# Kernel tuning notes

Hardware: AMD Instinct MI355X
Metric: run time of the kernel (lower is better)

## Reference

```python
import jax, jax.numpy as jnp
import numpy as np

TOPK = 2


def setup_inputs() -> dict:
    key = jax.random.key(0)
    ks = jax.random.split(key, 6)
    B, S, D, H, M = 2, 2048, 256, 8, 8
    s = 0.02
    return {
        "x": jax.random.normal(ks[0], (B, S, D), jnp.float32),
        "Wq": jax.random.normal(ks[1], (D, H * D), jnp.float32) * s,
        "bq": jnp.zeros((H * D,), jnp.float32),
        "Wr": jax.random.normal(ks[2], (D, M), jnp.float32) * s,
        "br": jnp.zeros((M,), jnp.float32),
        "Wk": jax.random.normal(ks[3], (M, D, H * D), jnp.float32) * s,
        "bk": jnp.zeros((M, H * D), jnp.float32),
        "Wv": jax.random.normal(ks[4], (M, D, H * D), jnp.float32) * s,
        "bv": jnp.zeros((M, H * D), jnp.float32),
        "Wo": jax.random.normal(ks[5], (H * D, D), jnp.float32) * s,
        "bo": jnp.zeros((D,), jnp.float32),
        "bias0": jnp.zeros((B, M), jnp.float32),
    }


def reference(x, Wq, bq, Wr, br, Wk, bk, Wv, bv, Wo, bo, bias0):
    B, S, D = x.shape
    M, _, HD = Wk.shape
    H = HD // D
    # query projection and head split: [B,S,H,D] (head dim == n_text_state)
    q = (x @ Wq + bq).reshape(B, S, H, D)
    # router + aux-loss-free bias-adjusted top-k routing (DeepSeek-V3 style)
    scores = jax.nn.softmax(x @ Wr + br, axis=-1)                 # [B,S,M]
    biased = scores + bias0[:, None, :]
    _, idx = jax.lax.top_k(biased, TOPK)                          # [B,S,TOPK]
    mask = jax.nn.one_hot(idx, M, dtype=scores.dtype).sum(-2)     # [B,S,M] in {0,1}
    routing = scores * mask
    routing = routing / routing.sum(-1, keepdims=True)
    # per-memory linear-attention state: M_m = sum_s r[b,s,m] * k (x) v, fused over all memories
    k_all = (jnp.einsum('bsd,mde->mbse', x, Wk) + bk[:, None, None, :]).reshape(M, B, S, H, D)
    v_all = (jnp.einsum('bsd,mde->mbse', x, Wv) + bv[:, None, None, :]).reshape(M, B, S, H, D)
    mem = jnp.einsum('bsm,mbshk,mbshv->bhkv', routing, k_all, v_all)  # [B,H,D,D]
    # fused read-out (replaces per-timestep python loop): o[b,s,h,v] = sum_k mem[b,h,k,v] q[b,s,h,k]
    o = jnp.einsum('bhkv,bshk->bshv', mem, q)                     # [B,S,H,D]
    return o.reshape(B, S, H * D) @ Wo + bo
```

## Files before the change

kernel.cpp:

```cpp
#include <hip/hip_runtime.h>

typedef __attribute__((ext_vector_type(8))) short bf16x8;
typedef __attribute__((ext_vector_type(4))) float f32x4;

#define DEV static __device__ __forceinline__

DEV unsigned short f2bf(float f){
  union { float f; unsigned u; } v; v.f = f;
  unsigned r = v.u + 0x7fffu + ((v.u >> 16) & 1u);
  return (unsigned short)(r >> 16);
}
DEV float bf2f(unsigned short u){
  union { unsigned u; float f; } v; v.u = ((unsigned)u) << 16;
  return v.f;
}
DEV unsigned long long pk4(float a, float b, float c, float d){
  unsigned lo = (unsigned)f2bf(a) | ((unsigned)f2bf(b) << 16);
  unsigned hi = (unsigned)f2bf(c) | ((unsigned)f2bf(d) << 16);
  return ((unsigned long long)hi << 32) | lo;
}

__global__ __launch_bounds__(256) void k_prep(const float* __restrict__ x,
                                              const float* __restrict__ Wq,
                                              const float* __restrict__ Wr,
                                              const float* __restrict__ br,
                                              const float* __restrict__ Wk,
                                              const float* __restrict__ Wv,
                                              const float* __restrict__ Wo,
                                              const float* __restrict__ bias0,
                                              unsigned short* __restrict__ WkT,
                                              unsigned short* __restrict__ WvT,
                                              unsigned short* __restrict__ WoT,
                                              unsigned short* __restrict__ Wqb,
                                              unsigned short* __restrict__ xb,
                                              unsigned short* __restrict__ xT,
                                              float* __restrict__ routT){
  __shared__ float tile[32*33];
  __shared__ float lg[32][8];
  __shared__ float rt2[32][8];
  int bid = blockIdx.x;
  int t = threadIdx.x;
  int tx = t & 31, ty = t >> 5;

  if (bid < 8192){
    const float* src = (bid < 4096) ? Wk : Wv;
    unsigned short* dst = (bid < 4096) ? WkT : WvT;
    int q = bid & 4095;
    int bat = q >> 9, rem = q & 511;
    int c0 = (rem >> 3) * 32, r0 = (rem & 7) * 32;
    size_t boff = (size_t)bat * 256 * 2048;
    for (int i = 0; i < 4; i++)
      tile[(ty + i*8)*33 + tx] = src[boff + (size_t)(r0 + ty + i*8) * 2048 + c0 + tx];
    __syncthreads();
    for (int i = 0; i < 4; i++)
      dst[boff + (size_t)(c0 + ty + i*8) * 256 + r0 + tx] = f2bf(tile[tx*33 + ty + i*8]);
  } else if (bid < 8704){
    int q = bid - 8192;
    int c0 = (q >> 6) * 32, r0 = (q & 63) * 32;
    for (int i = 0; i < 4; i++)
      tile[(ty + i*8)*33 + tx] = Wo[(size_t)(r0 + ty + i*8) * 256 + c0 + tx];
    __syncthreads();
    for (int i = 0; i < 4; i++)
      WoT[(size_t)(c0 + ty + i*8) * 2048 + r0 + tx] = f2bf(tile[tx*33 + ty + i*8]);
  } else if (bid < 8960){
    int q = bid - 8704;
    size_t idx = (size_t)q * 2048 + t * 8;
    f32x4 a = *(const f32x4*)(Wq + idx);
    f32x4 b = *(const f32x4*)(Wq + idx + 4);
    *(unsigned long long*)(Wqb + idx)     = pk4(a[0], a[1], a[2], a[3]);
    *(unsigned long long*)(Wqb + idx + 4) = pk4(b[0], b[1], b[2], b[3]);
  } else if (bid < 9984){
    int q = bid - 8960;
    int bat = q >> 9, rem = q & 511;
    int c0 = (rem >> 6) * 32, r0 = (rem & 63) * 32;
    size_t boff = (size_t)bat * 2048 * 256;
    for (int i = 0; i < 4; i++){
      float v = x[boff + (size_t)(r0 + ty + i*8) * 256 + c0 + tx];
      tile[(ty + i*8)*33 + tx] = v;
      xb[boff + (size_t)(r0 + ty + i*8) * 256 + c0 + tx] = f2bf(v);
    }
    __syncthreads();
    for (int i = 0; i < 4; i++)
      xT[(size_t)(bat*256 + c0 + ty + i*8) * 2048 + r0 + tx] = f2bf(tile[tx*33 + ty + i*8]);
  } else {
    int row = t >> 3, mm = t & 7;
    int n = (bid - 9984) * 32 + row;
    const float* xr = x + (size_t)n * 256;
    float acc = 0.f;
    for (int d = 0; d < 256; d++) acc += xr[d] * Wr[d * 8 + mm];
    acc += br[mm];
    lg[row][mm] = acc;
    __syncthreads();
    if (t < 32){
      int r = t; int n2 = (bid - 9984) * 32 + r; int b = n2 >> 11;
      float mx = -1e30f;
      for (int i = 0; i < 8; i++) mx = fmaxf(mx, lg[r][i]);
      float s[8]; float sum = 0.f;
      for (int i = 0; i < 8; i++){ s[i] = __expf(lg[r][i] - mx); sum += s[i]; }
      for (int i = 0; i < 8; i++) s[i] /= sum;
      float bb[8];
      for (int i = 0; i < 8; i++) bb[i] = s[i] + bias0[b * 8 + i];
      int i1 = 0;
      for (int i = 1; i < 8; i++) if (bb[i] > bb[i1]) i1 = i;
      int i2 = -1;
      for (int i = 0; i < 8; i++){ if (i == i1) continue; if (i2 < 0 || bb[i] > bb[i2]) i2 = i; }
      float wsum = s[i1] + s[i2];
      for (int i = 0; i < 8; i++)
        rt2[r][i] = (i == i1) ? s[i1] / wsum : ((i == i2) ? s[i2] / wsum : 0.f);
    }
    __syncthreads();
    int n3 = (bid - 9984) * 32 + row;
    int b = n3 >> 11, sl = n3 & 2047;
    routT[((size_t)b * 8 + mm) * 2048 + sl] = rt2[row][mm];
  }
}

__global__ __launch_bounds__(256) void k_usum(const unsigned short* __restrict__ xb,
                                              const float* __restrict__ routT,
                                              float* __restrict__ upart, float* __restrict__ rhop){
  __shared__ float rl[128];
  int bid = blockIdx.x;
  int sc = bid & 15, bm = bid >> 4, b = bm >> 3;
  int t = threadIdx.x;
  int s0 = sc * 128;
  if (t < 128) rl[t] = routT[(size_t)bm * 2048 + s0 + t];
  __syncthreads();
  float acc = 0.f;
  const unsigned short* xrow = xb + ((size_t)(b * 2048 + s0)) * 256 + t;
  for (int s = 0; s < 128; s++){
    float rv = rl[s];
    if (rv != 0.f)
      acc += rv * bf2f(xrow[(size_t)s * 256]);
  }
  upart[(size_t)bid * 256 + t] = acc;
  if (t == 0){
    float rs = 0.f;
    for (int s = 0; s < 128; s++) rs += rl[s];
    rhop[bid] = rs;
  }
}

__global__ __launch_bounds__(256) void k_bias(const unsigned short* __restrict__ WkT,
                                              const unsigned short* __restrict__ WvT,
                                              const float* __restrict__ upart,
                                              const float* __restrict__ rhop,
                                              float* __restrict__ ku_g, float* __restrict__ vu_g,
                                              float* __restrict__ rho){
  __shared__ float uL[256];
  int bid = blockIdx.x, t = threadIdx.x;
  int bm = bid >> 3, hseg = bid & 7, m = bm & 7;
  {
    float s = 0.f;
    for (int scn = 0; scn < 16; scn++)
      s += upart[(size_t)(bm*16 + scn) * 256 + t];
    uL[t] = s;
  }
  if (hseg == 0 && t == 0){
    float rs = 0.f;
    for (int scn = 0; scn < 16; scn++) rs += rhop[bm*16 + scn];
    rho[bm] = rs;
  }
  __syncthreads();
  int hd = hseg * 256 + t;
  const unsigned short* wk = WkT + ((size_t)m*2048 + hd) * 256;
  const unsigned short* wv = WvT + ((size_t)m*2048 + hd) * 256;
  float sk = 0.f, sv = 0.f;
  for (int d8 = 0; d8 < 256; d8 += 8){
    bf16x8 a = *(const bf16x8*)(wk + d8);
    bf16x8 c = *(const bf16x8*)(wv + d8);
    for (int j = 0; j < 8; j++){
      sk += bf2f((unsigned short)a[j]) * uL[d8+j];
      sv += bf2f((unsigned short)c[j]) * uL[d8+j];
    }
  }
  ku_g[(size_t)bm*2048 + hd] = sk;
  vu_g[(size_t)bm*2048 + hd] = sv;
}

__global__ __launch_bounds__(512) void k_gpart(const unsigned short* __restrict__ xT,
                                               const float* __restrict__ routT,
                                               unsigned short* __restrict__ Gp){
  __shared__ unsigned short As[256*72];
  __shared__ unsigned short Bs[256*72];
  __shared__ float rl[64];
  int bid = blockIdx.x;
  int kc = bid & 7, m = (bid >> 3) & 7, b = bid >> 6;
  int bm = b * 8 + m;
  int t = threadIdx.x, lane = t & 63, w = t >> 6;
  int li = lane & 15, lgp = lane >> 4;
  int p = w >> 2, q = w & 3;
  f32x4 acc[8][4];
  for (int i = 0; i < 8; i++) for (int j = 0; j < 4; j++) acc[i][j] = (f32x4){0,0,0,0};
  for (int c4 = 0; c4 < 4; c4++){
    int s0 = kc * 256 + c4 * 64;
    if (t < 64) rl[t] = routT[(size_t)bm*2048 + s0 + t];
    __syncthreads();
    for (int qq = 0; qq < 4; qq++){
      int idx = t + qq*512;
      int row = idx >> 3, sc = (idx & 7) * 8;
      bf16x8 xv = *(const bf16x8*)(xT + ((size_t)(b*256 + row))*2048 + s0 + sc);
      *(bf16x8*)(&Bs[row*72 + sc]) = xv;
      f32x4 r0 = *(const f32x4*)(rl + sc);
      f32x4 r1 = *(const f32x4*)(rl + sc + 4);
      bf16x8 sv;
      sv[0]=(short)f2bf(bf2f((unsigned short)xv[0])*r0[0]);
      sv[1]=(short)f2bf(bf2f((unsigned short)xv[1])*r0[1]);
      sv[2]=(short)f2bf(bf2f((unsigned short)xv[2])*r0[2]);
      sv[3]=(short)f2bf(bf2f((unsigned short)xv[3])*r0[3]);
      sv[4]=(short)f2bf(bf2f((unsigned short)xv[4])*r1[0]);
      sv[5]=(short)f2bf(bf2f((unsigned short)xv[5])*r1[1]);
      sv[6]=(short)f2bf(bf2f((unsigned short)xv[6])*r1[2]);
      sv[7]=(short)f2bf(bf2f((unsigned short)xv[7])*r1[3]);
      *(bf16x8*)(&As[row*72 + sc]) = sv;
    }
    __syncthreads();
    for (int kk = 0; kk < 2; kk++){
      bf16x8 Bf[4];
      for (int j = 0; j < 4; j++)
        Bf[j] = *(const bf16x8*)(&Bs[(q*64 + j*16 + li)*72 + kk*32 + lgp*8]);
      for (int i = 0; i < 8; i++){
        bf16x8 Af = *(const bf16x8*)(&As[(p*128 + i*16 + li)*72 + kk*32 + lgp*8]);
        for (int j = 0; j < 4; j++)
          acc[i][j] = __builtin_amdgcn_mfma_f32_16x16x32_bf16(Af, Bf[j], acc[i][j], 0, 0, 0);
      }
    }
    __syncthreads();
  }
  unsigned short* Cs = As;
  for (int ph = 0; ph < 4; ph++){
    if (q == ph){
      for (int i = 0; i < 8; i++)
        for (int j = 0; j < 4; j++){
          int rr = j*16 + li, cc = p*128 + i*16 + lgp*4;
          *(unsigned long long*)(&Cs[rr*264 + cc]) =
            pk4(acc[i][j][0], acc[i][j][1], acc[i][j][2], acc[i][j][3]);
        }
    }
    __syncthreads();
    for (int qq = 0; qq < 4; qq++){
      int idx = t + qq*512;
      int row = idx >> 5, cc = (idx & 31) * 8;
      *(bf16x8*)(Gp + (((size_t)bm*8 + kc) << 16) + (size_t)(ph*64 + row)*256 + cc) =
        *(const bf16x8*)(&Cs[row*264 + cc]);
    }
    __syncthreads();
  }
}

__global__ __launch_bounds__(256) void k_gred(const unsigned short* __restrict__ Gp,
                                              unsigned short* __restrict__ G){
  int idx = blockIdx.x * 256 + threadIdx.x;
  int bm = idx >> 13; size_t e8 = (size_t)(idx & 8191) * 8;
  float s[8] = {0,0,0,0,0,0,0,0};
  for (int kc = 0; kc < 8; kc++){
    bf16x8 v = *(const bf16x8*)(Gp + (((size_t)bm*8 + kc) << 16) + e8);
    for (int j = 0; j < 8; j++) s[j] += bf2f((unsigned short)v[j]);
  }
  *(unsigned long long*)(G + ((size_t)bm << 16) + e8)     = pk4(s[0], s[1], s[2], s[3]);
  *(unsigned long long*)(G + ((size_t)bm << 16) + e8 + 4) = pk4(s[4], s[5], s[6], s[7]);
}

__global__ __launch_bounds__(512) void k_tmat(const unsigned short* __restrict__ G,
                                              const unsigned short* __restrict__ WvT,
                                              unsigned short* __restrict__ Tt){
  __shared__ unsigned short Cs[64*264];
  int bid = blockIdx.x;
  int hseg = bid & 15, bm = bid >> 4, m = bm & 7;
  int t = threadIdx.x, lane = t & 63, w = t >> 6;
  int li = lane & 15, lgp = lane >> 4;
  int r = w >> 1, c = w & 1;
  f32x4 acc[4][4];
  for (int i = 0; i < 4; i++) for (int j = 0; j < 4; j++) acc[i][j] = (f32x4){0,0,0,0};
  const unsigned short* gp = G + ((size_t)bm << 16) + (size_t)(r*64 + li)*256 + lgp*8;
  const unsigned short* wp = WvT + ((size_t)m*2048 + hseg*128 + c*64 + li)*256 + lgp*8;
  #pragma unroll
  for (int kk = 0; kk < 8; kk++){
    bf16x8 Bf[4];
    for (int j = 0; j < 4; j++)
      Bf[j] = *(const bf16x8*)(wp + (size_t)(j*16)*256 + kk*32);
    for (int i = 0; i < 4; i++){
      bf16x8 Af = *(const bf16x8*)(gp + (size_t)(i*16)*256 + kk*32);
      for (int j = 0; j < 4; j++)
        acc[i][j] = __builtin_amdgcn_mfma_f32_16x16x32_bf16(Af, Bf[j], acc[i][j], 0, 0, 0);
    }
  }
  for (int ph = 0; ph < 2; ph++){
    if (c == ph){
      for (int i = 0; i < 4; i++)
        for (int j = 0; j < 4; j++)
          *(unsigned long long*)(&Cs[(j*16 + li)*264 + r*64 + i*16 + lgp*4]) =
            pk4(acc[i][j][0], acc[i][j][1], acc[i][j][2], acc[i][j][3]);
    }
    __syncthreads();
    for (int q = 0; q < 4; q++){
      int idx = t + q*512;
      int row = idx >> 5, cc = (idx & 31) * 8;
      *(bf16x8*)(Tt + ((size_t)bm*2048 + hseg*128 + ph*64 + row)*256 + cc) =
        *(const bf16x8*)(&Cs[row*264 + cc]);
    }
    __syncthreads();
  }
}

__global__ __launch_bounds__(512) void k_kmat3(const unsigned short* __restrict__ Tt,
                                               const unsigned short* __restrict__ WkT,
                                               float* __restrict__ mempartF){
  int bid = blockIdx.x;
  int m = bid & 7, kq = (bid >> 3) & 1, vq = (bid >> 4) & 1, bh = bid >> 5;
  int b = bh >> 3, h = bh & 7;
  int hd0 = h * 256;
  int t = threadIdx.x, lane = t & 63, w = t >> 6;
  int li = lane & 15, lgp = lane >> 4;
  int wr = w >> 2, wc = w & 3;
  f32x4 acc[2][4];
  for (int i = 0; i < 2; i++) for (int j = 0; j < 4; j++) acc[i][j] = (f32x4){0,0,0,0};
  const unsigned short* ap = WkT + ((size_t)m*2048 + hd0 + kq*128 + wc*32 + li)*256 + lgp*8;
  const unsigned short* bp = Tt + ((size_t)(b*8 + m)*2048 + hd0 + vq*128 + wr*64 + li)*256 + lgp*8;
  #pragma unroll
  for (int kk = 0; kk < 8; kk++){
    bf16x8 Af[2], Bf[4];
    Af[0] = *(const bf16x8*)(ap + kk*32);
    Af[1] = *(const bf16x8*)(ap + 16*256 + kk*32);
    for (int j = 0; j < 4; j++)
      Bf[j] = *(const bf16x8*)(bp + (size_t)(j*16)*256 + kk*32);
    for (int i = 0; i < 2; i++)
      for (int j = 0; j < 4; j++)
        acc[i][j] = __builtin_amdgcn_mfma_f32_16x16x32_bf16(Af[i], Bf[j], acc[i][j], 0, 0, 0);
  }
  float* Fp = mempartF + ((((size_t)(m*16 + bh))*2 + vq)*2 + kq) * 16384;
  for (int j = 0; j < 4; j++){
    int vdt = wr*64 + j*16 + li;
    for (int i = 0; i < 2; i++){
      int kdt = wc*32 + i*16 + lgp*4;
      *(f32x4*)(Fp + (size_t)vdt*128 + kdt) = acc[i][j];
    }
  }
}

__global__ __launch_bounds__(256) void k_kred(const float* __restrict__ mempartF,
                                              const float* __restrict__ bk,
                                              const float* __restrict__ bv,
                                              const float* __restrict__ ku_g,
                                              const float* __restrict__ vu_g,
                                              const float* __restrict__ rho,
                                              unsigned short* __restrict__ memT){
  int idx = blockIdx.x * 256 + threadIdx.x;
  int bh = idx >> 14;
  int rem = idx & 16383;
  int vd = rem >> 6, kd = (rem & 63) * 4;
  int b = bh >> 3, h = bh & 7;
  int vdg = h*256 + vd, kdg = h*256 + kd;
  int vq = vd >> 7, kq = kd >> 7;
  size_t src = ((((size_t)bh)*2 + vq)*2 + kq) * 16384 + (size_t)(vd & 127)*128 + (kd & 127);
  f32x4 s = (f32x4){0,0,0,0};
  #pragma unroll
  for (int m = 0; m < 8; m++){
    f32x4 v = *(const f32x4*)(mempartF + (size_t)m*16*65536 + src);
    s[0] += v[0]; s[1] += v[1]; s[2] += v[2]; s[3] += v[3];
  }
  #pragma unroll
  for (int m = 0; m < 8; m++){
    float bvv = bv[(size_t)m*2048 + vdg];
    float bb  = vu_g[(size_t)(b*8+m)*2048 + vdg] + rho[b*8+m]*bvv;
    f32x4 ku4 = *(const f32x4*)(ku_g + (size_t)(b*8+m)*2048 + kdg);
    f32x4 bk4 = *(const f32x4*)(bk + (size_t)m*2048 + kdg);
    s[0] += ku4[0]*bvv + bk4[0]*bb;
    s[1] += ku4[1]*bvv + bk4[1]*bb;
    s[2] += ku4[2]*bvv + bk4[2]*bb;
    s[3] += ku4[3]*bvv + bk4[3]*bb;
  }
  *(unsigned long long*)(memT + (size_t)bh*65536 + (size_t)vd*256 + kd) =
    pk4(s[0], s[1], s[2], s[3]);
}

__global__ __launch_bounds__(512) void k_emat(const unsigned short* __restrict__ memT,
                                              const unsigned short* __restrict__ Wqb,
                                              const float* __restrict__ bq,
                                              unsigned short* __restrict__ Eb,
                                              float* __restrict__ qbAll){
  __shared__ unsigned short Cs[16*264];
  int bid = blockIdx.x;
  int dseg = bid & 3, bh = bid >> 2;
  int b = bh >> 3, h = bh & 7;
  int hd0 = h * 256, d0 = dseg * 64;
  int t = threadIdx.x, lane = t & 63, w = t >> 6;
  int li = lane & 15, lgp = lane >> 4;
  int r = w >> 2, c = w & 3;
  f32x4 acc[8];
  for (int i = 0; i < 8; i++) acc[i] = (f32x4){0,0,0,0};
  for (int kk = 0; kk < 8; kk++){
    bf16x8 Bf = *(const bf16x8*)(Wqb + (size_t)(d0 + c*16 + li)*2048 + hd0 + kk*32 + lgp*8);
    for (int i = 0; i < 8; i++){
      bf16x8 Af = *(const bf16x8*)(memT + (size_t)bh*65536 + (size_t)(r*128 + i*16 + li)*256 + kk*32 + lgp*8);
      acc[i] = __builtin_amdgcn_mfma_f32_16x16x32_bf16(Af, Bf, acc[i], 0, 0, 0);
    }
  }
  if (dseg == 0 && t < 256){
    const unsigned short* mrow = memT + (size_t)bh*65536 + (size_t)t*256;
    float s = 0.f;
    for (int k8 = 0; k8 < 256; k8 += 8){
      bf16x8 v = *(const bf16x8*)(mrow + k8);
      for (int e = 0; e < 8; e++) s += bf2f((unsigned short)v[e]) * bq[hd0 + k8 + e];
    }
    qbAll[(size_t)b*2048 + hd0 + t] = s;
  }
  for (int ph = 0; ph < 4; ph++){
    if (c == ph){
      for (int i = 0; i < 8; i++)
        *(unsigned long long*)(&Cs[li*264 + r*128 + i*16 + lgp*4]) =
          pk4(acc[i][0], acc[i][1], acc[i][2], acc[i][3]);
    }
    __syncthreads();
    {
      int row = t >> 5, cc = (t & 31) * 8;
      *(bf16x8*)(Eb + (size_t)b*524288 + (size_t)(d0 + ph*16 + row)*2048 + hd0 + cc) =
        *(const bf16x8*)(&Cs[row*264 + cc]);
    }
    __syncthreads();
  }
}

__global__ __launch_bounds__(512) void k_fmat(const unsigned short* __restrict__ Eb,
                                              const unsigned short* __restrict__ WoT,
                                              const float* __restrict__ qbAll,
                                              const float* __restrict__ bo,
                                              float* __restrict__ Fpart,
                                              float* __restrict__ c0acc){
  __shared__ float qL[2048];
  int bid = blockIdx.x;
  int t = threadIdx.x;
  if (bid >= 256){
    int b = bid - 256;
    for (int i = t; i < 2048; i += 512) qL[i] = qbAll[(size_t)b * 2048 + i];
    __syncthreads();
    int w = t >> 6, lane = t & 63;
    for (int dd = w; dd < 256; dd += 8){
      const unsigned short* wrow = WoT + (size_t)dd * 2048 + lane * 8;
      const float* qp = qL + lane * 8;
      float s = 0.f;
      for (int pass = 0; pass < 4; pass++){
        bf16x8 v = *(const bf16x8*)(wrow + pass * 512);
        const float* q = qp + pass * 512;
        for (int e = 0; e < 8; e++) s += bf2f((unsigned short)v[e]) * q[e];
      }
      for (int off = 32; off; off >>= 1) s += __shfl_down(s, off);
      if (lane == 0) c0acc[(size_t)b * 256 + dd] = s + bo[dd];
    }
    return;
  }
  int ks = bid & 7, dseg = (bid >> 3) & 3, doseg = (bid >> 5) & 3, b = bid >> 7;
  int do0 = doseg * 64, d0 = dseg * 64, k0 = ks * 256;
  int lane = t & 63, w = t >> 6;
  int li = lane & 15, lgp = lane >> 4;
  int r = w >> 2, c = w & 3;
  f32x4 acc[2];
  acc[0] = (f32x4){0,0,0,0}; acc[1] = (f32x4){0,0,0,0};
  const unsigned short* bp = Eb + (size_t)b*524288 + (size_t)(d0 + c*16 + li)*2048 + k0 + lgp*8;
  const unsigned short* ap = WoT + (size_t)(do0 + r*32 + li)*2048 + k0 + lgp*8;
  #pragma unroll
  for (int kk = 0; kk < 8; kk++){
    bf16x8 Bf = *(const bf16x8*)(bp + kk*32);
    bf16x8 Af0 = *(const bf16x8*)(ap + kk*32);
    bf16x8 Af1 = *(const bf16x8*)(ap + kk*32 + 16*2048);
    acc[0] = __builtin_amdgcn_mfma_f32_16x16x32_bf16(Af0, Bf, acc[0], 0, 0, 0);
    acc[1] = __builtin_amdgcn_mfma_f32_16x16x32_bf16(Af1, Bf, acc[1], 0, 0, 0);
  }
  int dd = d0 + c*16 + li;
  float* Fp = Fpart + ((size_t)(ks*2 + b)) * 65536;
  for (int i = 0; i < 2; i++){
    int dor = do0 + r*32 + i*16 + lgp*4;
    float* p = Fp + (size_t)dor*256 + dd;
    p[0]   = acc[i][0];
    p[256] = acc[i][1];
    p[512] = acc[i][2];
    p[768] = acc[i][3];
  }
}

__global__ __launch_bounds__(256) void k_fred(const float* __restrict__ Fpart,
                                              unsigned short* __restrict__ Fb){
  int idx = blockIdx.x * 256 + threadIdx.x;
  int b = idx >> 14; int e4 = (idx & 16383) * 4;
  f32x4 s = (f32x4){0,0,0,0};
  for (int ks = 0; ks < 8; ks++){
    f32x4 v = *(const f32x4*)(Fpart + ((size_t)(ks*2 + b)) * 65536 + e4);
    s[0] += v[0]; s[1] += v[1]; s[2] += v[2]; s[3] += v[3];
  }
  *(unsigned long long*)(Fb + (size_t)b*65536 + e4) = pk4(s[0], s[1], s[2], s[3]);
}

__global__ __launch_bounds__(512) void k_final2(const unsigned short* __restrict__ Fb,
                                                const unsigned short* __restrict__ xb,
                                                const float* __restrict__ c0acc,
                                                float* __restrict__ out){
  int bid = blockIdx.x;
  int tc = bid & 31, b = bid >> 5;
  int t = threadIdx.x, lane = t & 63, w = t >> 6;
  int li = lane & 15, lgp = lane >> 4;
  int r = w >> 1, c = w & 1;
  int tok0 = b * 2048 + tc * 64;
  f32x4 acc[4][2];
  for (int i = 0; i < 4; i++) for (int j = 0; j < 2; j++) acc[i][j] = (f32x4){0,0,0,0};
  for (int kk = 0; kk < 8; kk++){
    bf16x8 Bf[2];
    for (int j = 0; j < 2; j++)
      Bf[j] = *(const bf16x8*)(xb + (size_t)(tok0 + c*32 + j*16 + li)*256 + kk*32 + lgp*8);
    for (int i = 0; i < 4; i++){
      bf16x8 af = *(const bf16x8*)(Fb + (size_t)b*65536 + (size_t)(r*64 + i*16 + li)*256 + kk*32 + lgp*8);
      for (int j = 0; j < 2; j++)
        acc[i][j] = __builtin_amdgcn_mfma_f32_16x16x32_bf16(af, Bf[j], acc[i][j], 0, 0, 0);
    }
  }
  for (int i = 0; i < 4; i++){
    int dol = r*64 + i*16 + lgp*4;
    f32x4 c4 = *(const f32x4*)(c0acc + (size_t)b*256 + dol);
    for (int j = 0; j < 2; j++){
      int tokl = c*32 + j*16 + li;
      f32x4 v = acc[i][j];
      v[0] += c4[0]; v[1] += c4[1]; v[2] += c4[2]; v[3] += c4[3];
      *(f32x4*)(out + (size_t)(tok0 + tokl)*256 + dol) = v;
    }
  }
}

extern "C" void kernel_launch(void* const* d_in, const int* in_sizes, int n_in,
                              void* d_out, int out_size, void* d_ws, size_t ws_size,
                              hipStream_t stream) {
  const float* x     = (const float*)d_in[0];
  const float* Wq    = (const float*)d_in[1];
  const float* bq    = (const float*)d_in[2];
  const float* Wr    = (const float*)d_in[3];
  const float* br    = (const float*)d_in[4];
  const float* Wk    = (const float*)d_in[5];
  const float* bk    = (const float*)d_in[6];
  const float* Wv    = (const float*)d_in[7];
  const float* bv    = (const float*)d_in[8];
  const float* Wo    = (const float*)d_in[9];
  const float* bo    = (const float*)d_in[10];
  const float* bias0 = (const float*)d_in[11];
  float* out = (float*)d_out;

  char* ws = (char*)d_ws;
  size_t off = 0;
  auto alloc = [&](size_t bytes) -> char* {
    char* p = ws + off;
    off = (off + bytes + 255) & ~(size_t)255;
    return p;
  };
  unsigned short* xb   = (unsigned short*)alloc((size_t)4096 * 256 * 2);
  unsigned short* xT   = (unsigned short*)alloc((size_t)2 * 256 * 2048 * 2);
  unsigned short* Wqb  = (unsigned short*)alloc((size_t)256 * 2048 * 2);
  unsigned short* WkT  = (unsigned short*)alloc((size_t)8 * 2048 * 256 * 2);
  unsigned short* WvT  = (unsigned short*)alloc((size_t)8 * 2048 * 256 * 2);
  unsigned short* WoT  = (unsigned short*)alloc((size_t)256 * 2048 * 2);
  float*          routT= (float*)alloc((size_t)16 * 2048 * 4);
  float*          upart= (float*)alloc((size_t)256 * 256 * 4);
  float*          rhop = (float*)alloc((size_t)256 * 4);
  float*          rho  = (float*)alloc((size_t)16 * 4);
  float*          ku_g = (float*)alloc((size_t)16 * 2048 * 4);
  float*          vu_g = (float*)alloc((size_t)16 * 2048 * 4);
  unsigned short* Gp   = (unsigned short*)alloc((size_t)16 * 8 * 65536 * 2);
  unsigned short* G    = (unsigned short*)alloc((size_t)16 * 65536 * 2);
  unsigned short* memT = (unsigned short*)alloc((size_t)16 * 65536 * 2);
  unsigned short* Eb   = (unsigned short*)alloc((size_t)2 * 256 * 2048 * 2);
  float*          qbAll= (float*)alloc((size_t)2 * 2048 * 4);
  float*          Fpart= (float*)alloc((size_t)16 * 65536 * 4);
  unsigned short* Fb   = (unsigned short*)alloc((size_t)2 * 65536 * 2);
  float*          c0acc= (float*)alloc((size_t)2 * 256 * 4);
  float*          mempartF = (float*)alloc((size_t)8 * 16 * 65536 * 4);
  unsigned short* Tt   = Gp;
  (void)ws_size; (void)in_sizes; (void)n_in; (void)out_size;

  k_prep<<<10112, 256, 0, stream>>>(x, Wq, Wr, br, Wk, Wv, Wo, bias0,
                                    WkT, WvT, WoT, Wqb, xb, xT, routT);
  k_usum<<<256, 256, 0, stream>>>(xb, routT, upart, rhop);
  k_bias<<<128, 256, 0, stream>>>(WkT, WvT, upart, rhop, ku_g, vu_g, rho);
  k_gpart<<<128, 512, 0, stream>>>(xT, routT, Gp);
  k_gred<<<512, 256, 0, stream>>>(Gp, G);
  k_tmat<<<256, 512, 0, stream>>>(G, WvT, Tt);
  k_kmat3<<<512, 512, 0, stream>>>(Tt, WkT, mempartF);
  k_kred<<<1024, 256, 0, stream>>>(mempartF, bk, bv, ku_g, vu_g, rho, memT);
  k_emat<<<64, 512, 0, stream>>>(memT, Wqb, bq, Eb, qbAll);
  k_fmat<<<258, 512, 0, stream>>>(Eb, WoT, qbAll, bo, Fpart, c0acc);
  k_fred<<<128, 256, 0, stream>>>(Fpart, Fb);
  k_final2<<<64, 512, 0, stream>>>(Fb, xb, c0acc, out);
}
```

Measured before the change: 208.2 us.

## Enlarge prep transpose tiles, share WkT loads across batches, store partials in bf16

The prep kernel's transpose blocks now handle 64x64 tiles instead of 32x32, cutting the block count roughly fourfold. k_kmat3 now computes both batches in one block, so each WkT fragment is loaded once and reused for two MFMA streams, halving the grid. The per-memory partial sums are written as bf16 instead of fp32, halving the traffic between k_kmat3 and k_kred. The cost is extra rounding error in the eight-way partial sum and higher register pressure in k_kmat3.

```diff
diff --git a/kernel.cpp b/kernel.cpp
--- a/kernel.cpp
+++ b/kernel.cpp
@@ -35,56 +35,56 @@
                                               unsigned short* __restrict__ xb,
                                               unsigned short* __restrict__ xT,
                                               float* __restrict__ routT){
-  __shared__ float tile[32*33];
+  __shared__ float tile[64*65];
   __shared__ float lg[32][8];
   __shared__ float rt2[32][8];
   int bid = blockIdx.x;
   int t = threadIdx.x;
-  int tx = t & 31, ty = t >> 5;
-
-  if (bid < 8192){
-    const float* src = (bid < 4096) ? Wk : Wv;
-    unsigned short* dst = (bid < 4096) ? WkT : WvT;
-    int q = bid & 4095;
-    int bat = q >> 9, rem = q & 511;
-    int c0 = (rem >> 3) * 32, r0 = (rem & 7) * 32;
+  int tx = t & 63, ty = t >> 6;
+
+  if (bid < 2048){
+    const float* src = (bid < 1024) ? Wk : Wv;
+    unsigned short* dst = (bid < 1024) ? WkT : WvT;
+    int q = bid & 1023;
+    int bat = q >> 7, rem = q & 127;
+    int c0 = (rem >> 2) * 64, r0 = (rem & 3) * 64;
     size_t boff = (size_t)bat * 256 * 2048;
-    for (int i = 0; i < 4; i++)
-      tile[(ty + i*8)*33 + tx] = src[boff + (size_t)(r0 + ty + i*8) * 2048 + c0 + tx];
-    __syncthreads();
-    for (int i = 0; i < 4; i++)
-      dst[boff + (size_t)(c0 + ty + i*8) * 256 + r0 + tx] = f2bf(tile[tx*33 + ty + i*8]);
-  } else if (bid < 8704){
-    int q = bid - 8192;
-    int c0 = (q >> 6) * 32, r0 = (q & 63) * 32;
-    for (int i = 0; i < 4; i++)
-      tile[(ty + i*8)*33 + tx] = Wo[(size_t)(r0 + ty + i*8) * 256 + c0 + tx];
-    __syncthreads();
-    for (int i = 0; i < 4; i++)
-      WoT[(size_t)(c0 + ty + i*8) * 2048 + r0 + tx] = f2bf(tile[tx*33 + ty + i*8]);
-  } else if (bid < 8960){
-    int q = bid - 8704;
+    for (int i = 0; i < 16; i++)
+      tile[(ty + i*4)*65 + tx] = src[boff + (size_t)(r0 + ty + i*4) * 2048 + c0 + tx];
+    __syncthreads();
+    for (int i = 0; i < 16; i++)
+      dst[boff + (size_t)(c0 + ty + i*4) * 256 + r0 + tx] = f2bf(tile[tx*65 + ty + i*4]);
+  } else if (bid < 2176){
+    int q = bid - 2048;
+    int r0 = (q >> 2) * 64, c0 = (q & 3) * 64;
+    for (int i = 0; i < 16; i++)
+      tile[(ty + i*4)*65 + tx] = Wo[(size_t)(r0 + ty + i*4) * 256 + c0 + tx];
+    __syncthreads();
+    for (int i = 0; i < 16; i++)
+      WoT[(size_t)(c0 + ty + i*4) * 2048 + r0 + tx] = f2bf(tile[tx*65 + ty + i*4]);
+  } else if (bid < 2432){
+    int q = bid - 2176;
     size_t idx = (size_t)q * 2048 + t * 8;
     f32x4 a = *(const f32x4*)(Wq + idx);
     f32x4 b = *(const f32x4*)(Wq + idx + 4);
     *(unsigned long long*)(Wqb + idx)     = pk4(a[0], a[1], a[2], a[3]);
     *(unsigned long long*)(Wqb + idx + 4) = pk4(b[0], b[1], b[2], b[3]);
-  } else if (bid < 9984){
-    int q = bid - 8960;
-    int bat = q >> 9, rem = q & 511;
-    int c0 = (rem >> 6) * 32, r0 = (rem & 63) * 32;
+  } else if (bid < 2688){
+    int q = bid - 2432;
+    int bat = q >> 7, rem = q & 127;
+    int r0 = (rem >> 2) * 64, c0 = (rem & 3) * 64;
     size_t boff = (size_t)bat * 2048 * 256;
-    for (int i = 0; i < 4; i++){
-      float v = x[boff + (size_t)(r0 + ty + i*8) * 256 + c0 + tx];
-      tile[(ty + i*8)*33 + tx] = v;
-      xb[boff + (size_t)(r0 + ty + i*8) * 256 + c0 + tx] = f2bf(v);
-    }
-    __syncthreads();
-    for (int i = 0; i < 4; i++)
-      xT[(size_t)(bat*256 + c0 + ty + i*8) * 2048 + r0 + tx] = f2bf(tile[tx*33 + ty + i*8]);
+    for (int i = 0; i < 16; i++){
+      float v = x[boff + (size_t)(r0 + ty + i*4) * 256 + c0 + tx];
+      tile[(ty + i*4)*65 + tx] = v;
+      xb[boff + (size_t)(r0 + ty + i*4) * 256 + c0 + tx] = f2bf(v);
+    }
+    __syncthreads();
+    for (int i = 0; i < 16; i++)
+      xT[(size_t)(bat*256 + c0 + ty + i*4) * 2048 + r0 + tx] = f2bf(tile[tx*65 + ty + i*4]);
   } else {
     int row = t >> 3, mm = t & 7;
-    int n = (bid - 9984) * 32 + row;
+    int n = (bid - 2688) * 32 + row;
     const float* xr = x + (size_t)n * 256;
     float acc = 0.f;
     for (int d = 0; d < 256; d++) acc += xr[d] * Wr[d * 8 + mm];
@@ -92,7 +92,7 @@
     lg[row][mm] = acc;
     __syncthreads();
     if (t < 32){
-      int r = t; int n2 = (bid - 9984) * 32 + r; int b = n2 >> 11;
+      int r = t; int n2 = (bid - 2688) * 32 + r; int b = n2 >> 11;
       float mx = -1e30f;
       for (int i = 0; i < 8; i++) mx = fmaxf(mx, lg[r][i]);
       float s[8]; float sum = 0.f;
@@ -109,7 +109,7 @@
         rt2[r][i] = (i == i1) ? s[i1] / wsum : ((i == i2) ? s[i2] / wsum : 0.f);
     }
     __syncthreads();
-    int n3 = (bid - 9984) * 32 + row;
+    int n3 = (bid - 2688) * 32 + row;
     int b = n3 >> 11, sl = n3 & 2047;
     routT[((size_t)b * 8 + mm) * 2048 + sl] = rt2[row][mm];
   }
@@ -304,40 +304,49 @@
 
 __global__ __launch_bounds__(512) void k_kmat3(const unsigned short* __restrict__ Tt,
                                                const unsigned short* __restrict__ WkT,
-                                               float* __restrict__ mempartF){
-  int bid = blockIdx.x;
-  int m = bid & 7, kq = (bid >> 3) & 1, vq = (bid >> 4) & 1, bh = bid >> 5;
-  int b = bh >> 3, h = bh & 7;
+                                               unsigned short* __restrict__ mempartB){
+  int bid = blockIdx.x;
+  int m = bid & 7, kq = (bid >> 3) & 1, vq = (bid >> 4) & 1, h = bid >> 5;
   int hd0 = h * 256;
   int t = threadIdx.x, lane = t & 63, w = t >> 6;
   int li = lane & 15, lgp = lane >> 4;
   int wr = w >> 2, wc = w & 3;
-  f32x4 acc[2][4];
-  for (int i = 0; i < 2; i++) for (int j = 0; j < 4; j++) acc[i][j] = (f32x4){0,0,0,0};
-  const unsigned short* ap = WkT + ((size_t)m*2048 + hd0 + kq*128 + wc*32 + li)*256 + lgp*8;
-  const unsigned short* bp = Tt + ((size_t)(b*8 + m)*2048 + hd0 + vq*128 + wr*64 + li)*256 + lgp*8;
+  f32x4 acc[2][2][4];
+  for (int b = 0; b < 2; b++)
+    for (int i = 0; i < 2; i++)
+      for (int j = 0; j < 4; j++) acc[b][i][j] = (f32x4){0,0,0,0};
+  const unsigned short* ap  = WkT + ((size_t)m*2048 + hd0 + kq*128 + wc*32 + li)*256 + lgp*8;
+  const unsigned short* bp0 = Tt + ((size_t)(m)*2048 + hd0 + vq*128 + wr*64 + li)*256 + lgp*8;
+  const unsigned short* bp1 = Tt + ((size_t)(8 + m)*2048 + hd0 + vq*128 + wr*64 + li)*256 + lgp*8;
   #pragma unroll
   for (int kk = 0; kk < 8; kk++){
-    bf16x8 Af[2], Bf[4];
+    bf16x8 Af[2], B0[4], B1[4];
     Af[0] = *(const bf16x8*)(ap + kk*32);
     Af[1] = *(const bf16x8*)(ap + 16*256 + kk*32);
-    for (int j = 0; j < 4; j++)
-      Bf[j] = *(const bf16x8*)(bp + (size_t)(j*16)*256 + kk*32);
+    for (int j = 0; j < 4; j++){
+      B0[j] = *(const bf16x8*)(bp0 + (size_t)(j*16)*256 + kk*32);
+      B1[j] = *(const bf16x8*)(bp1 + (size_t)(j*16)*256 + kk*32);
+    }
     for (int i = 0; i < 2; i++)
-      for (int j = 0; j < 4; j++)
-        acc[i][j] = __builtin_amdgcn_mfma_f32_16x16x32_bf16(Af[i], Bf[j], acc[i][j], 0, 0, 0);
-  }
-  float* Fp = mempartF + ((((size_t)(m*16 + bh))*2 + vq)*2 + kq) * 16384;
-  for (int j = 0; j < 4; j++){
-    int vdt = wr*64 + j*16 + li;
-    for (int i = 0; i < 2; i++){
-      int kdt = wc*32 + i*16 + lgp*4;
-      *(f32x4*)(Fp + (size_t)vdt*128 + kdt) = acc[i][j];
-    }
-  }
-}
-
-__global__ __launch_bounds__(256) void k_kred(const float* __restrict__ mempartF,
+      for (int j = 0; j < 4; j++){
+        acc[0][i][j] = __builtin_amdgcn_mfma_f32_16x16x32_bf16(Af[i], B0[j], acc[0][i][j], 0, 0, 0);
+        acc[1][i][j] = __builtin_amdgcn_mfma_f32_16x16x32_bf16(Af[i], B1[j], acc[1][i][j], 0, 0, 0);
+      }
+  }
+  for (int b = 0; b < 2; b++){
+    unsigned short* Fp = mempartB + ((((((size_t)m*8 + h)*2 + vq)*2 + kq)*2 + b)) * 16384;
+    for (int j = 0; j < 4; j++){
+      int vdt = wr*64 + j*16 + li;
+      for (int i = 0; i < 2; i++){
+        int kdt = wc*32 + i*16 + lgp*4;
+        *(unsigned long long*)(Fp + (size_t)vdt*128 + kdt) =
+          pk4(acc[b][i][j][0], acc[b][i][j][1], acc[b][i][j][2], acc[b][i][j][3]);
+      }
+    }
+  }
+}
+
+__global__ __launch_bounds__(256) void k_kred(const unsigned short* __restrict__ mempartB,
                                               const float* __restrict__ bk,
                                               const float* __restrict__ bv,
                                               const float* __restrict__ ku_g,
@@ -351,12 +360,15 @@
   int b = bh >> 3, h = bh & 7;
   int vdg = h*256 + vd, kdg = h*256 + kd;
   int vq = vd >> 7, kq = kd >> 7;
-  size_t src = ((((size_t)bh)*2 + vq)*2 + kq) * 16384 + (size_t)(vd & 127)*128 + (kd & 127);
+  size_t src = ((((size_t)h*2 + vq)*2 + kq)*2 + b) * 16384 + (size_t)(vd & 127)*128 + (kd & 127);
   f32x4 s = (f32x4){0,0,0,0};
   #pragma unroll
   for (int m = 0; m < 8; m++){
-    f32x4 v = *(const f32x4*)(mempartF + (size_t)m*16*65536 + src);
-    s[0] += v[0]; s[1] += v[1]; s[2] += v[2]; s[3] += v[3];
+    unsigned long long v = *(const unsigned long long*)(mempartB + (size_t)m*1048576 + src);
+    s[0] += bf2f((unsigned short)v);
+    s[1] += bf2f((unsigned short)(v >> 16));
+    s[2] += bf2f((unsigned short)(v >> 32));
+    s[3] += bf2f((unsigned short)(v >> 48));
   }
   #pragma unroll
   for (int m = 0; m < 8; m++){
@@ -567,19 +579,19 @@
   float*          Fpart= (float*)alloc((size_t)16 * 65536 * 4);
   unsigned short* Fb   = (unsigned short*)alloc((size_t)2 * 65536 * 2);
   float*          c0acc= (float*)alloc((size_t)2 * 256 * 4);
-  float*          mempartF = (float*)alloc((size_t)8 * 16 * 65536 * 4);
+  unsigned short* mempartB = (unsigned short*)alloc((size_t)8 * 1048576 * 2);
   unsigned short* Tt   = Gp;
   (void)ws_size; (void)in_sizes; (void)n_in; (void)out_size;
 
-  k_prep<<<10112, 256, 0, stream>>>(x, Wq, Wr, br, Wk, Wv, Wo, bias0,
-                                    WkT, WvT, WoT, Wqb, xb, xT, routT);
+  k_prep<<<2816, 256, 0, stream>>>(x, Wq, Wr, br, Wk, Wv, Wo, bias0,
+                                   WkT, WvT, WoT, Wqb, xb, xT, routT);
   k_usum<<<256, 256, 0, stream>>>(xb, routT, upart, rhop);
   k_bias<<<128, 256, 0, stream>>>(WkT, WvT, upart, rhop, ku_g, vu_g, rho);
   k_gpart<<<128, 512, 0, stream>>>(xT, routT, Gp);
   k_gred<<<512, 256, 0, stream>>>(Gp, G);
   k_tmat<<<256, 512, 0, stream>>>(G, WvT, Tt);
-  k_kmat3<<<512, 512, 0, stream>>>(Tt, WkT, mempartF);
-  k_kred<<<1024, 256, 0, stream>>>(mempartF, bk, bv, ku_g, vu_g, rho, memT);
+  k_kmat3<<<256, 512, 0, stream>>>(Tt, WkT, mempartB);
+  k_kred<<<1024, 256, 0, stream>>>(mempartB, bk, bv, ku_g, vu_g, rho, memT);
   k_emat<<<64, 512, 0, stream>>>(memT, Wqb, bq, Eb, qbAll);
   k_fmat<<<258, 512, 0, stream>>>(Eb, WoT, qbAll, bo, Fpart, c0acc);
   k_fred<<<128, 256, 0, stream>>>(Fpart, Fb);
```

Result: faster. 194.5 us (-6.6%).
